# Kernel optimization log

Hardware: AMD Instinct MI355X
Metric: run time of the kernel (lower is better)

The kernel has to match this reference:

```python
import jax, jax.numpy as jnp
import numpy as np

CTX_WIN = 5
PAD = (CTX_WIN - 1) // 2


def setup_inputs() -> dict:
    key = jax.random.key(0)
    k1, k2, k3 = jax.random.split(key, 3)
    B, S, H, A = 64, 1024, 128, 8
    return {
        "batch_docIn": jax.random.normal(k1, (B, S, H), dtype=jnp.float32),
        "aspEmbed_weight": jax.random.uniform(k2, (A, CTX_WIN * H), dtype=jnp.float32, minval=-0.01, maxval=0.01),
        "aspProj": jax.random.uniform(k3, (A, H, H), dtype=jnp.float32, minval=-0.01, maxval=0.01),
    }


def reference(batch_docIn, aspEmbed_weight, aspProj):
    B, S, H = batch_docIn.shape
    A = aspProj.shape[0]
    # Per-aspect projection: (A, B, S, H)
    proj = jnp.einsum('bsh,ahf->absf', batch_docIn, aspProj)
    E = aspEmbed_weight.reshape(A, H, CTX_WIN)
    # Zero-pad along seq, then accumulate windowed scores without materializing
    padded = jnp.pad(proj, ((0, 0), (0, 0), (PAD, PAD), (0, 0)))
    attn = sum(
        jnp.einsum('absh,ah->abs',
                   jax.lax.dynamic_slice_in_dim(padded, w, S, axis=2),
                   E[:, :, w])
        for w in range(CTX_WIN)
    )  # (A, B, S)
    attn = jax.nn.softmax(attn, axis=2)  # softmax over seq (torch dim=1)
    rep = jnp.einsum('absh,abs->abh', proj, attn)  # (A, B, H)
    # outputs: attn (B, A, S), rep (B, A, H)
    return attn.transpose(1, 0, 2), rep.transpose(1, 0, 2)
```

## Files before the change

kernel.cpp:

```cpp
#include <hip/hip_runtime.h>
#include <hip/hip_bf16.h>

#define S_DIM 1024
#define H_DIM 128
#define A_DIM 8
#define W_WIN 5

typedef unsigned int uint;
typedef unsigned short ushort;
typedef __attribute__((ext_vector_type(8))) short short8;
typedef __attribute__((ext_vector_type(4))) float f32x4;

union U128 { uint4 u; short8 s; };

__device__ __forceinline__ ushort f2bf(float f) {
    uint u = __float_as_uint(f);
    uint r = (u + 0x7fffu + ((u >> 16) & 1u)) >> 16;
    return (ushort)r;
}

__global__ __launch_bounds__(128) void k_g(const float* __restrict__ P,
                                           const float* __restrict__ We,
                                           ushort* __restrict__ Gt) {
    const int a = blockIdx.x;
    const int h = threadIdx.x;
    if (a >= A_DIM) {
        for (int i = h; i < W_WIN * H_DIM; i += 128) Gt[a * (W_WIN * H_DIM) + i] = 0;
        return;
    }
    __shared__ float Es[H_DIM * W_WIN];
    for (int i = h; i < H_DIM * W_WIN; i += 128) Es[i] = We[a * (H_DIM * W_WIN) + i];
    __syncthreads();

    const float* Pr = P + ((size_t)a * H_DIM + h) * H_DIM;
    float acc[W_WIN] = {0.f, 0.f, 0.f, 0.f, 0.f};
#pragma unroll 8
    for (int f = 0; f < H_DIM; f += 4) {
        float4 pv = *(const float4*)(Pr + f);
        float pj[4] = {pv.x, pv.y, pv.z, pv.w};
#pragma unroll
        for (int j = 0; j < 4; ++j) {
            const float p = pj[j];
            const float* e = &Es[(f + j) * W_WIN];
#pragma unroll
            for (int w = 0; w < W_WIN; ++w) acc[w] += p * e[w];
        }
    }
#pragma unroll
    for (int w = 0; w < W_WIN; ++w)
        Gt[a * (W_WIN * H_DIM) + w * H_DIM + h] = f2bf(acc[w]);
}

#define CS 64
#define RROWS (CS + 4)
#define GPAD 81
__global__ __launch_bounds__(256) void k_scores(const float* __restrict__ Din,
                                                const ushort* __restrict__ Gt,
                                                float* __restrict__ score) {
    __shared__ uint4 Dl[RROWS * 16];
    __shared__ uint4 Gl[16 * GPAD];
    const int b  = blockIdx.y;
    const int s0 = blockIdx.x * CS;
    const int t  = threadIdx.x;
    const float* Db = Din + (size_t)b * S_DIM * H_DIM;

    for (int i = t; i < RROWS * 16; i += 256) {
        const int r = i >> 4, c = i & 15;
        const int gs = s0 - 2 + r;
        float4 va = make_float4(0.f, 0.f, 0.f, 0.f), vb = va;
        if (gs >= 0 && gs < S_DIM) {
            const float* p = Db + (size_t)gs * H_DIM + c * 8;
            va = ((const float4*)p)[0];
            vb = ((const float4*)p)[1];
        }
        uint4 q;
        q.x = (uint)f2bf(va.x) | ((uint)f2bf(va.y) << 16);
        q.y = (uint)f2bf(va.z) | ((uint)f2bf(va.w) << 16);
        q.z = (uint)f2bf(vb.x) | ((uint)f2bf(vb.y) << 16);
        q.w = (uint)f2bf(vb.z) | ((uint)f2bf(vb.w) << 16);
        Dl[r * 16 + (c ^ (r & 15))] = q;
    }
    {
        const uint4* Gg = (const uint4*)Gt;
        for (int i = t; i < 16 * 80; i += 256) {
            const int n = i / 80, c = i - n * 80;
            Gl[n * GPAD + c] = Gg[i];
        }
    }
    __syncthreads();

    const int lane = t & 63;
    const int wv   = t >> 6;
    const int lm   = lane & 15;
    const int lq   = lane >> 4;
    const int smBase = wv * 16;

    f32x4 acc = {0.f, 0.f, 0.f, 0.f};
#pragma unroll
    for (int kk = 0; kk < 20; ++kk) {
        const int w = kk >> 2;
        const int r = smBase + lm + w;
        const int cidx = (kk & 3) * 4 + lq;
        U128 av, bv;
        av.u = Dl[r * 16 + (cidx ^ (r & 15))];
        bv.u = Gl[lm * GPAD + kk * 4 + lq];
        acc = __builtin_amdgcn_mfma_f32_16x16x32_bf16(av.s, bv.s, acc, 0, 0, 0);
    }

    const int n = lm;
    if (n < A_DIM) {
        float* op = score + (((size_t)b * A_DIM + n) * S_DIM) + s0 + smBase + lq * 4;
        *(f32x4*)op = acc;
    }
}

__global__ __launch_bounds__(256) void k_softmax(const float* __restrict__ score,
                                                 float* __restrict__ attn) {
    const int row = blockIdx.x;
    const int t = threadIdx.x;
    __shared__ float red[8];
    const float* sp = score + (size_t)row * S_DIM;
    float4 v = *(const float4*)(sp + t * 4);
    float m = fmaxf(fmaxf(v.x, v.y), fmaxf(v.z, v.w));
#pragma unroll
    for (int off = 32; off > 0; off >>= 1) m = fmaxf(m, __shfl_xor(m, off));
    if ((t & 63) == 0) red[t >> 6] = m;
    __syncthreads();
    m = fmaxf(fmaxf(red[0], red[1]), fmaxf(red[2], red[3]));
    float4 e;
    e.x = __expf(v.x - m); e.y = __expf(v.y - m);
    e.z = __expf(v.z - m); e.w = __expf(v.w - m);
    float sum = e.x + e.y + e.z + e.w;
#pragma unroll
    for (int off = 32; off > 0; off >>= 1) sum += __shfl_xor(sum, off);
    if ((t & 63) == 0) red[4 + (t >> 6)] = sum;
    __syncthreads();
    const float rz = 1.0f / (red[4] + red[5] + red[6] + red[7]);
    e.x *= rz; e.y *= rz; e.z *= rz; e.w *= rz;
    *(float4*)(attn + (size_t)row * S_DIM + t * 4) = e;
}

__global__ __launch_bounds__(256) void k_wsum(const float* __restrict__ Din,
                                              const float* __restrict__ attn,
                                              float* __restrict__ wsP) {
    const int slc = blockIdx.x;
    const int b = blockIdx.y;
    const int t = threadIdx.x;
    const int h = t & 127;
    const int half = __builtin_amdgcn_readfirstlane(t >> 7);
    const int s0 = slc * 128 + half * 64;

    const float* dp = Din + ((size_t)b * S_DIM + s0) * H_DIM + h;
    float dreg[64];
#pragma unroll
    for (int i = 0; i < 64; ++i) dreg[i] = dp[(size_t)i * H_DIM];

    const float* ap = attn + (size_t)b * A_DIM * S_DIM + s0;
    float* wp = wsP + ((size_t)(b * 16 + slc * 2 + half) * A_DIM) * H_DIM + h;
#pragma unroll
    for (int a = 0; a < A_DIM; ++a) {
        const float* aa = ap + (size_t)a * S_DIM;
        float acc = 0.f;
#pragma unroll
        for (int i = 0; i < 64; ++i) acc += aa[i] * dreg[i];
        wp[(size_t)a * H_DIM] = acc;
    }
}

__global__ __launch_bounds__(128) void k_rep(const float* __restrict__ wsP,
                                             const float* __restrict__ P,
                                             float* __restrict__ rep) {
    __shared__ float ws[H_DIM];
    const int ba = blockIdx.x;
    const int b = ba >> 3, a = ba & 7;
    const int t = threadIdx.x;
    float s = 0.f;
#pragma unroll
    for (int k = 0; k < 16; ++k)
        s += wsP[(((size_t)(b * 16 + k)) * A_DIM + a) * H_DIM + t];
    ws[t] = s;
    __syncthreads();
    const float* Pa = P + (size_t)a * H_DIM * H_DIM + t;
    float acc = 0.f;
#pragma unroll 32
    for (int hh = 0; hh < H_DIM; ++hh)
        acc += ws[hh] * Pa[(size_t)hh * H_DIM];
    rep[(size_t)ba * H_DIM + t] = acc;
}

extern "C" void kernel_launch(void* const* d_in, const int* in_sizes, int n_in,
                              void* d_out, int out_size, void* d_ws, size_t ws_size,
                              hipStream_t stream) {
    const float* docIn = (const float*)d_in[0];
    const float* We    = (const float*)d_in[1];
    const float* P     = (const float*)d_in[2];
    float* out = (float*)d_out;

    const int B = in_sizes[0] / (S_DIM * H_DIM);

    ushort* Gt   = (ushort*)d_ws;
    float* score = (float*)((char*)d_ws + 32768);
    float* wsP   = score + (size_t)B * A_DIM * S_DIM;

    k_g<<<16, 128, 0, stream>>>(P, We, Gt);
    k_scores<<<dim3(S_DIM / CS, B), 256, 0, stream>>>(docIn, Gt, score);
    k_softmax<<<B * A_DIM, 256, 0, stream>>>(score, out);
    k_wsum<<<dim3(S_DIM / 128, B), 256, 0, stream>>>(docIn, out, wsP);
    k_rep<<<B * A_DIM, 128, 0, stream>>>(wsP, P, out + (size_t)B * A_DIM * S_DIM);
}
```

Before: 107.5 us.

## Fuse softmax into score and weighted-sum kernels via atomic exp-sum

Removes the separate softmax kernel. The score kernel now accumulates per-row sums of exp(score) through shared and global atomics into a buffer that k_g zeroes. The weighted-sum kernel normalizes with 1/Z, writes attn, and reads the probabilities from LDS instead of global memory. The score tile also grows to 128 rows, with two MFMA accumulators per wave. Skipping max subtraction risks overflow for large scores and makes the result depend on atomic ordering, and each wsum block now also has to read its score tile.

```diff
diff --git a/kernel.cpp b/kernel.cpp
--- a/kernel.cpp
+++ b/kernel.cpp
@@ -21,11 +21,13 @@
 
 __global__ __launch_bounds__(128) void k_g(const float* __restrict__ P,
                                            const float* __restrict__ We,
-                                           ushort* __restrict__ Gt) {
+                                           ushort* __restrict__ Gt,
+                                           float* __restrict__ Z, int nZ) {
     const int a = blockIdx.x;
     const int h = threadIdx.x;
     if (a >= A_DIM) {
         for (int i = h; i < W_WIN * H_DIM; i += 128) Gt[a * (W_WIN * H_DIM) + i] = 0;
+        if (a == A_DIM) for (int i = h; i < nZ; i += 128) Z[i] = 0.f;
         return;
     }
     __shared__ float Es[H_DIM * W_WIN];
@@ -51,14 +53,16 @@
         Gt[a * (W_WIN * H_DIM) + w * H_DIM + h] = f2bf(acc[w]);
 }
 
-#define CS 64
+#define CS 128
 #define RROWS (CS + 4)
 #define GPAD 81
 __global__ __launch_bounds__(256) void k_scores(const float* __restrict__ Din,
                                                 const ushort* __restrict__ Gt,
-                                                float* __restrict__ score) {
+                                                float* __restrict__ score,
+                                                float* __restrict__ Z) {
     __shared__ uint4 Dl[RROWS * 16];
     __shared__ uint4 Gl[16 * GPAD];
+    __shared__ float Zl[8];
     const int b  = blockIdx.y;
     const int s0 = blockIdx.x * CS;
     const int t  = threadIdx.x;
@@ -87,65 +91,69 @@
             Gl[n * GPAD + c] = Gg[i];
         }
     }
+    if (t < 8) Zl[t] = 0.f;
     __syncthreads();
 
     const int lane = t & 63;
     const int wv   = t >> 6;
     const int lm   = lane & 15;
     const int lq   = lane >> 4;
-    const int smBase = wv * 16;
-
-    f32x4 acc = {0.f, 0.f, 0.f, 0.f};
+
+    f32x4 acc0 = {0.f, 0.f, 0.f, 0.f};
+    f32x4 acc1 = {0.f, 0.f, 0.f, 0.f};
 #pragma unroll
     for (int kk = 0; kk < 20; ++kk) {
         const int w = kk >> 2;
-        const int r = smBase + lm + w;
+        const int r0 = wv * 16 + lm + w;
         const int cidx = (kk & 3) * 4 + lq;
-        U128 av, bv;
-        av.u = Dl[r * 16 + (cidx ^ (r & 15))];
-        bv.u = Gl[lm * GPAD + kk * 4 + lq];
-        acc = __builtin_amdgcn_mfma_f32_16x16x32_bf16(av.s, bv.s, acc, 0, 0, 0);
+        const int cx = cidx ^ (r0 & 15);
+        U128 av0, av1, bv;
+        bv.u  = Gl[lm * GPAD + kk * 4 + lq];
+        av0.u = Dl[r0 * 16 + cx];
+        av1.u = Dl[(r0 + 64) * 16 + cx];
+        acc0 = __builtin_amdgcn_mfma_f32_16x16x32_bf16(av0.s, bv.s, acc0, 0, 0, 0);
+        acc1 = __builtin_amdgcn_mfma_f32_16x16x32_bf16(av1.s, bv.s, acc1, 0, 0, 0);
     }
 
     const int n = lm;
     if (n < A_DIM) {
-        float* op = score + (((size_t)b * A_DIM + n) * S_DIM) + s0 + smBase + lq * 4;
-        *(f32x4*)op = acc;
-    }
-}
-
-__global__ __launch_bounds__(256) void k_softmax(const float* __restrict__ score,
-                                                 float* __restrict__ attn) {
-    const int row = blockIdx.x;
-    const int t = threadIdx.x;
-    __shared__ float red[8];
-    const float* sp = score + (size_t)row * S_DIM;
-    float4 v = *(const float4*)(sp + t * 4);
-    float m = fmaxf(fmaxf(v.x, v.y), fmaxf(v.z, v.w));
-#pragma unroll
-    for (int off = 32; off > 0; off >>= 1) m = fmaxf(m, __shfl_xor(m, off));
-    if ((t & 63) == 0) red[t >> 6] = m;
-    __syncthreads();
-    m = fmaxf(fmaxf(red[0], red[1]), fmaxf(red[2], red[3]));
-    float4 e;
-    e.x = __expf(v.x - m); e.y = __expf(v.y - m);
-    e.z = __expf(v.z - m); e.w = __expf(v.w - m);
-    float sum = e.x + e.y + e.z + e.w;
-#pragma unroll
-    for (int off = 32; off > 0; off >>= 1) sum += __shfl_xor(sum, off);
-    if ((t & 63) == 0) red[4 + (t >> 6)] = sum;
-    __syncthreads();
-    const float rz = 1.0f / (red[4] + red[5] + red[6] + red[7]);
-    e.x *= rz; e.y *= rz; e.z *= rz; e.w *= rz;
-    *(float4*)(attn + (size_t)row * S_DIM + t * 4) = e;
+        float* op = score + (((size_t)b * A_DIM + n) * S_DIM) + s0 + wv * 16 + lq * 4;
+        *(f32x4*)op = acc0;
+        *(f32x4*)(op + 64) = acc1;
+    }
+
+    float es = __expf(acc0.x) + __expf(acc0.y) + __expf(acc0.z) + __expf(acc0.w)
+             + __expf(acc1.x) + __expf(acc1.y) + __expf(acc1.z) + __expf(acc1.w);
+    es += __shfl_xor(es, 16);
+    es += __shfl_xor(es, 32);
+    if ((lane & 48) == 0 && lm < A_DIM) atomicAdd(&Zl[lm], es);
+    __syncthreads();
+    if (t < A_DIM) atomicAdd(&Z[b * A_DIM + t], Zl[t]);
 }
 
 __global__ __launch_bounds__(256) void k_wsum(const float* __restrict__ Din,
-                                              const float* __restrict__ attn,
+                                              const float* __restrict__ score,
+                                              const float* __restrict__ Z,
+                                              float* __restrict__ attn,
                                               float* __restrict__ wsP) {
+    __shared__ float el[A_DIM * 128];
     const int slc = blockIdx.x;
     const int b = blockIdx.y;
     const int t = threadIdx.x;
+
+    {
+        const int a = t >> 5, s4 = (t & 31) << 2;
+        const float rz = 1.0f / Z[b * A_DIM + a];
+        const size_t off = ((size_t)b * A_DIM + a) * S_DIM + slc * 128 + s4;
+        float4 v = *(const float4*)(score + off);
+        float4 e;
+        e.x = __expf(v.x) * rz; e.y = __expf(v.y) * rz;
+        e.z = __expf(v.z) * rz; e.w = __expf(v.w) * rz;
+        *(float4*)(attn + off) = e;
+        *(float4*)(&el[a * 128 + s4]) = e;
+    }
+    __syncthreads();
+
     const int h = t & 127;
     const int half = __builtin_amdgcn_readfirstlane(t >> 7);
     const int s0 = slc * 128 + half * 64;
@@ -155,11 +163,10 @@
 #pragma unroll
     for (int i = 0; i < 64; ++i) dreg[i] = dp[(size_t)i * H_DIM];
 
-    const float* ap = attn + (size_t)b * A_DIM * S_DIM + s0;
     float* wp = wsP + ((size_t)(b * 16 + slc * 2 + half) * A_DIM) * H_DIM + h;
 #pragma unroll
     for (int a = 0; a < A_DIM; ++a) {
-        const float* aa = ap + (size_t)a * S_DIM;
+        const float* aa = &el[a * 128 + half * 64];
         float acc = 0.f;
 #pragma unroll
         for (int i = 0; i < 64; ++i) acc += aa[i] * dreg[i];
@@ -199,12 +206,12 @@
     const int B = in_sizes[0] / (S_DIM * H_DIM);
 
     ushort* Gt   = (ushort*)d_ws;
+    float* Z     = (float*)((char*)d_ws + 24576);
     float* score = (float*)((char*)d_ws + 32768);
     float* wsP   = score + (size_t)B * A_DIM * S_DIM;
 
-    k_g<<<16, 128, 0, stream>>>(P, We, Gt);
-    k_scores<<<dim3(S_DIM / CS, B), 256, 0, stream>>>(docIn, Gt, score);
-    k_softmax<<<B * A_DIM, 256, 0, stream>>>(score, out);
-    k_wsum<<<dim3(S_DIM / 128, B), 256, 0, stream>>>(docIn, out, wsP);
+    k_g<<<16, 128, 0, stream>>>(P, We, Gt, Z, B * A_DIM);
+    k_scores<<<dim3(S_DIM / CS, B), 256, 0, stream>>>(docIn, Gt, score, Z);
+    k_wsum<<<dim3(S_DIM / 128, B), 256, 0, stream>>>(docIn, score, Z, out, wsP);
     k_rep<<<B * A_DIM, 128, 0, stream>>>(wsP, P, out + (size_t)B * A_DIM * S_DIM);
 }
```

After: 96.50 us. 1.11x faster.
